# Performance work log

Hardware: AMD Instinct MI355X
Metric: run time of the kernel (lower is better)

Reference implementation:

```python
import jax, jax.numpy as jnp
import numpy as np

PATCH = 16
FEAT = 64
RADIUS = 3
EPS = 1e-06


def setup_inputs() -> dict:
    key = jax.random.key(0)
    ks = jax.random.split(key, 7)
    B, G, H, W, N = 8, 20, 512, 512, 32
    HE = jax.random.uniform(ks[0], (B, 3, H, W), jnp.float32)
    HQST = jax.random.uniform(ks[1], (B, G, H, W), jnp.float32)
    cell_mask = jax.random.randint(ks[2], (B, N, H, W), 0, 2, jnp.int32)
    w1 = jax.random.normal(ks[3], (FEAT, FEAT), jnp.float32) * 0.05
    b1 = jax.random.normal(ks[4], (FEAT,), jnp.float32) * 0.05
    w2 = jax.random.normal(ks[5], (FEAT, FEAT), jnp.float32) * 0.05
    b2 = jax.random.normal(ks[6], (FEAT,), jnp.float32) * 0.05
    return dict(HE=HE, HQST=HQST, cell_mask=cell_mask, w1=w1, b1=b1, w2=w2, b2=b2)


def _select_patch(HE):
    # vectorized per-16x16-patch Shannon entropy + argmax (replaces nested python loops)
    B, _, H, W = HE.shape
    nh, nw = H // PATCH, W // PATCH
    Np = nh * nw
    gray = 0.2989 * HE[:, 0] + 0.587 * HE[:, 1] + 0.114 * HE[:, 2]  # [B,H,W]
    pat = gray.reshape(B, nh, PATCH, nw, PATCH).transpose(0, 1, 3, 2, 4).reshape(B, Np, PATCH * PATCH)
    pat = pat - pat.min(axis=-1, keepdims=True)
    v = pat / (pat.max(axis=-1, keepdims=True) + 1e-08)
    bins = jnp.clip((v * 256.0).astype(jnp.int32), 0, 255)          # 256-bin histc over [0,1]
    flat = (jnp.arange(B * Np, dtype=jnp.int32).reshape(B, Np, 1) * 256 + bins).reshape(-1)
    counts = jnp.zeros(B * Np * 256, jnp.float32).at[flat].add(1.0).reshape(B, Np, 256)
    prob = counts / (counts.sum(axis=-1, keepdims=True) + 1e-08)
    ent = -jnp.sum(jnp.where(prob > 0, prob * jnp.log2(jnp.where(prob > 0, prob, 1.0)), 0.0), axis=-1)
    idx = jnp.argmax(ent, axis=-1)
    return idx // nw, idx % nw


def _corr(X):
    # stabilized cell-cell correlation (detached in the original -> stop_gradient)
    X = X - X.mean(axis=0, keepdims=True)
    X = X / (jnp.std(X, axis=0, keepdims=True, ddof=1) + EPS)
    corr = X @ X.T / (X.shape[1] - 1)
    return jax.lax.stop_gradient(jnp.clip(corr, -1.0, 1.0))


def _ssim(x, y, C1=0.0001, C2=0.0001):
    mu_x, mu_y = x.mean(), y.mean()
    sx, sy = jnp.var(x, ddof=1), jnp.var(y, ddof=1)
    sxy = ((x - mu_x) * (y - mu_y)).mean()
    return (2 * mu_x * mu_y + C1) * (2 * sxy + C2) / ((mu_x ** 2 + mu_y ** 2 + C1) * (sx + sy + C2))


def reference(HE, HQST, cell_mask, w1, b1, w2, b2):
    row, col = _select_patch(HE)  # [B], [B]
    ax = jnp.arange(PATCH, dtype=jnp.float32)

    def per_image(he, hq, mask, r, c):
        y0, x0 = r * PATCH, c * PATCH
        he_c = jax.lax.dynamic_slice(he, (0, y0, x0), (he.shape[0], PATCH, PATCH))
        hq_c = jax.lax.dynamic_slice(hq, (0, y0, x0), (hq.shape[0], PATCH, PATCH))
        m = jax.lax.dynamic_slice(mask, (0, y0, x0), (mask.shape[0], PATCH, PATCH)).astype(jnp.float32)
        mn = m / (m.sum(axis=(1, 2), keepdims=True) + EPS)           # [N,P,P] normalized masks
        E_HE = jnp.einsum('chw,nhw->nc', he_c, mn)                   # [N,3]
        E_HQ = jnp.einsum('ghw,nhw->ng', hq_c, mn)                   # [N,G]
        ind = (m > 0).astype(jnp.float32)
        cnt = ind.sum(axis=(1, 2))
        cx = (ind * ax[None, None, :]).sum(axis=(1, 2)) / cnt        # mean x of nonzero pixels
        cy = (ind * ax[None, :, None]).sum(axis=(1, 2)) / cnt        # mean y
        coords = jnp.stack([cx, cy], axis=1)                         # [N,2]
        d2 = jnp.sum((coords[:, None, :] - coords[None, :, :]) ** 2, axis=-1)
        dist = jnp.sqrt(jnp.maximum(d2, 0.0))
        adj = jnp.exp(-dist / (RADIUS + EPS))
        adj = adj / (adj.sum(axis=1, keepdims=True) + 1e-08)
        pad_he = jnp.pad(E_HE, ((0, 0), (0, FEAT - E_HE.shape[1])))
        pad_hq = jnp.pad(E_HQ, ((0, 0), (0, FEAT - E_HQ.shape[1])))

        def gnn(X):
            h = jax.nn.relu((adj @ X) @ w1.T + b1)
            return jax.nn.relu((adj @ h) @ w2.T + b2)

        f_he = jnp.concatenate([pad_he, gnn(pad_he)], axis=1)        # [N,2*FEAT]
        f_hq = jnp.concatenate([pad_hq, gnn(pad_hq)], axis=1)
        ssim = jnp.clip(_ssim(_corr(f_he), _corr(f_hq)), 0.0, 1.0)
        return 1.0 - ssim

    losses = jax.vmap(per_image)(HE, HQST, cell_mask, row, col)
    return losses.sum() / HE.shape[0]
```

## Files before the change

kernel.cpp:

```cpp
#include <hip/hip_runtime.h>

#define IMG_W   512
#define IMG_HW  (512*512)
#define PATCH   16
#define NPATCH  1024
#define NCELL   32
#define NG      20
#define FEAT    64
#define EPSF    1e-6f

typedef unsigned long long ull;

__device__ __forceinline__ float wave_sum(float v) {
    #pragma unroll
    for (int o = 1; o < 64; o <<= 1) v += __shfl_xor(v, o, 64);
    return v;
}

__device__ __forceinline__ float block_sum(float v, float* sP, int t) {
    #pragma unroll
    for (int o = 1; o < 64; o <<= 1) v += __shfl_xor(v, o, 64);
    __syncthreads();
    if ((t & 63) == 0) sP[t >> 6] = v;
    __syncthreads();
    return sP[0] + sP[1] + sP[2] + sP[3];
}

__global__ __launch_bounds__(256) void k_entropy(const float* __restrict__ HE,
                                                 float* __restrict__ ent) {
    __shared__ int hist[4][256];
    int t = threadIdx.x;
    int w = t >> 6, l = t & 63;
    int pid = blockIdx.x * 4 + w;
    int b  = pid >> 10;
    int p  = pid & 1023;
    int pr = p >> 5, pc = p & 31;
    int r  = l >> 2, q = l & 3;
    size_t base = (size_t)b * 3 * IMG_HW
                + (size_t)(pr * PATCH + r) * IMG_W + pc * PATCH + q * 4;
    float4 cr = *(const float4*)(HE + base);
    float4 cg = *(const float4*)(HE + base + IMG_HW);
    float4 cb = *(const float4*)(HE + base + 2 * IMG_HW);
    float gray[4];
    gray[0] = __fadd_rn(__fadd_rn(__fmul_rn(0.2989f, cr.x), __fmul_rn(0.587f, cg.x)),
                        __fmul_rn(0.114f, cb.x));
    gray[1] = __fadd_rn(__fadd_rn(__fmul_rn(0.2989f, cr.y), __fmul_rn(0.587f, cg.y)),
                        __fmul_rn(0.114f, cb.y));
    gray[2] = __fadd_rn(__fadd_rn(__fmul_rn(0.2989f, cr.z), __fmul_rn(0.587f, cg.z)),
                        __fmul_rn(0.114f, cb.z));
    gray[3] = __fadd_rn(__fadd_rn(__fmul_rn(0.2989f, cr.w), __fmul_rn(0.587f, cg.w)),
                        __fmul_rn(0.114f, cb.w));
    float mn = fminf(fminf(gray[0], gray[1]), fminf(gray[2], gray[3]));
    float mx = fmaxf(fmaxf(gray[0], gray[1]), fmaxf(gray[2], gray[3]));
    #pragma unroll
    for (int o = 1; o < 64; o <<= 1) {
        mn = fminf(mn, __shfl_xor(mn, o, 64));
        mx = fmaxf(mx, __shfl_xor(mx, o, 64));
    }
    float denom = __fadd_rn(__fadd_rn(mx, -mn), 1e-8f);
    int* h = hist[w];
    h[l] = 0; h[l + 64] = 0; h[l + 128] = 0; h[l + 192] = 0;
    #pragma unroll
    for (int j = 0; j < 4; ++j) {
        float v = __fdiv_rn(__fadd_rn(gray[j], -mn), denom);
        int bin = (int)__fmul_rn(v, 256.0f);
        bin = min(max(bin, 0), 255);
        atomicAdd(&h[bin], 1);
    }
    float f[4];
    #pragma unroll
    for (int j = 0; j < 4; ++j) {
        int c = h[l + j * 64];
        float term = 0.0f;
        if (c > 0) {
            float prob = (float)c / 256.0f;
            term = prob * log2f(prob);
        }
        f[j] = term;
    }
    float s = __fadd_rn(__fadd_rn(f[0], f[2]), __fadd_rn(f[1], f[3]));
    #pragma unroll
    for (int o = 32; o >= 1; o >>= 1) s = __fadd_rn(s, __shfl_xor(s, o, 64));
    if (l == 0) ent[pid] = 0.0f - s;
}

__global__ __launch_bounds__(256) void k_argmax(const float* __restrict__ ent,
                                                int* __restrict__ bestp) {
    __shared__ ull sK[4];
    int t = threadIdx.x, b = blockIdx.x;
    ull best = 0ull;
    for (int i = t; i < NPATCH; i += 256) {
        float e = ent[b * NPATCH + i];
        ull k = ((ull)__float_as_uint(e) << 32)
              | (ull)(0xFFFFFFFFu - (unsigned)i);
        best = best > k ? best : k;
    }
    #pragma unroll
    for (int o = 1; o < 64; o <<= 1) {
        ull other = __shfl_xor(best, o, 64);
        best = best > other ? best : other;
    }
    if ((t & 63) == 0) sK[t >> 6] = best;
    __syncthreads();
    if (t == 0) {
        ull key = sK[0];
        #pragma unroll
        for (int wv = 1; wv < 4; ++wv) key = key > sK[wv] ? key : sK[wv];
        bestp[b] = (int)(0xFFFFFFFFu - (unsigned)(key & 0xFFFFFFFFull));
    }
}

__global__ __launch_bounds__(256) void k_moments(
    const float* __restrict__ HE, const float* __restrict__ HQ,
    const int*   __restrict__ M,  const int* __restrict__ bestp,
    float* __restrict__ feat)
{
    __shared__ __align__(16) float sM[256];
    __shared__ float sE[23];
    __shared__ float sP[3][4];
    int t = threadIdx.x;
    int b = blockIdx.x >> 5, n = blockIdx.x & 31;

    unsigned p = (unsigned)bestp[b];
    int y0 = (int)(p >> 5) * PATCH;
    int x0 = (int)(p & 31) * PATCH;
    int py = t >> 4, px = t & 15;
    size_t off = (size_t)(y0 + py) * IMG_W + (x0 + px);

    float mv = (float)M[((size_t)b * NCELL + n) * IMG_HW + off];
    sM[t] = mv;
    int w = t >> 6, lane = t & 63;
    float s0 = wave_sum(mv);
    float s1 = wave_sum(mv * (float)px);
    float s2 = wave_sum(mv * (float)py);
    if (lane == 0) { sP[0][w] = s0; sP[1][w] = s1; sP[2][w] = s2; }
    __syncthreads();

    int r = lane >> 2, q = lane & 3;
    size_t poff = (size_t)(y0 + r) * IMG_W + x0 + q * 4;
    float4 m4 = *(const float4*)&sM[r * 16 + q * 4];
    float part[6];
    #pragma unroll
    for (int kk = 0; kk < 6; ++kk) {
        int c = w + kk * 4;
        part[kk] = 0.0f;
        if (c < 23) {
            const float* cp = (c < 3) ? HE + ((size_t)b * 3 + c) * IMG_HW
                                      : HQ + ((size_t)b * NG + (c - 3)) * IMG_HW;
            float4 v = *(const float4*)(cp + poff);
            part[kk] = v.x * m4.x + v.y * m4.y + v.z * m4.z + v.w * m4.w;
        }
    }
    #pragma unroll
    for (int kk = 0; kk < 6; ++kk) {
        int c = w + kk * 4;
        if (c < 23) {
            float s = wave_sum(part[kk]);
            if (lane == 0) sE[c] = s;
        }
    }
    __syncthreads();
    if (t < 25) {
        float ms = sP[0][0] + sP[0][1] + sP[0][2] + sP[0][3];
        float s;
        if (t == 0)      s = (sP[1][0] + sP[1][1] + sP[1][2] + sP[1][3]) / ms;
        else if (t == 1) s = (sP[2][0] + sP[2][1] + sP[2][2] + sP[2][3]) / ms;
        else             s = sE[t - 2] / (ms + EPSF);
        feat[((size_t)b * 25 + t) * NCELL + n] = s;
    }
}

__global__ __launch_bounds__(256) void k_gnn(
    const float* __restrict__ w1, const float* __restrict__ b1,
    const float* __restrict__ w2, const float* __restrict__ b2,
    const float* __restrict__ feat, float* __restrict__ losses)
{
    __shared__ float sF[2][NCELL * 129];
    __shared__ float sU[4160];
    __shared__ float sAdj[NCELL * 33];
    __shared__ float sCx[32], sCy[32], sRow[32];
    __shared__ float sMu[128], sSd[128];
    __shared__ float sP[4];

    int t = threadIdx.x, b = blockIdx.x;
    const float* fb = feat + (size_t)b * 25 * NCELL;

    if (t < 32) { sCx[t] = fb[t]; sCy[t] = fb[NCELL + t]; }
    for (int i = t; i < 2 * NCELL * 129; i += 256) ((float*)sF)[i] = 0.0f;
    __syncthreads();

    for (int i = t; i < 23 * NCELL; i += 256) {
        int ch = i >> 5, n = i & 31;
        float v = fb[(2 + ch) * NCELL + n];
        if (ch < 3) sF[0][n * 129 + ch]       = v;
        else        sF[1][n * 129 + (ch - 3)] = v;
    }
    for (int i = t; i < NCELL * NCELL; i += 256) {
        int ii = i >> 5, jj = i & 31;
        float dx = sCx[ii] - sCx[jj], dy = sCy[ii] - sCy[jj];
        float dist = sqrtf(fmaxf(dx * dx + dy * dy, 0.0f));
        sAdj[ii * 33 + jj] = expf(-dist / (3.0f + EPSF));
    }
    __syncthreads();
    if (t < 32) {
        float s = 0.0f;
        #pragma unroll
        for (int j = 0; j < 32; ++j) s += sAdj[t * 33 + j];
        sRow[t] = s + 1e-8f;
    }
    __syncthreads();
    for (int i = t; i < NCELL * NCELL; i += 256)
        sAdj[(i >> 5) * 33 + (i & 31)] /= sRow[i >> 5];
    __syncthreads();

    float* sT = sU;
    float* sH = sU + 2080;
    for (int m = 0; m < 2; ++m) {
        float* F = sF[m];
        for (int idx = t; idx < NCELL * FEAT; idx += 256) {
            int n = idx >> 6, f = idx & 63;
            float s = 0.0f;
            #pragma unroll
            for (int k = 0; k < 32; ++k) s += sAdj[n * 33 + k] * F[k * 129 + f];
            sT[n * 65 + f] = s;
        }
        __syncthreads();
        for (int idx = t; idx < NCELL * FEAT; idx += 256) {
            int n = idx >> 6, f = idx & 63;
            const float4* wr = (const float4*)(w1 + (size_t)f * FEAT);
            const float*  tp = &sT[n * 65];
            float s = b1[f];
            #pragma unroll
            for (int k4 = 0; k4 < 16; ++k4) {
                float4 w4 = wr[k4];
                s += tp[k4*4+0]*w4.x + tp[k4*4+1]*w4.y + tp[k4*4+2]*w4.z + tp[k4*4+3]*w4.w;
            }
            sH[n * 65 + f] = fmaxf(s, 0.0f);
        }
        __syncthreads();
        for (int idx = t; idx < NCELL * FEAT; idx += 256) {
            int n = idx >> 6, f = idx & 63;
            float s = 0.0f;
            #pragma unroll
            for (int k = 0; k < 32; ++k) s += sAdj[n * 33 + k] * sH[k * 65 + f];
            sT[n * 65 + f] = s;
        }
        __syncthreads();
        for (int idx = t; idx < NCELL * FEAT; idx += 256) {
            int n = idx >> 6, f = idx & 63;
            const float4* wr = (const float4*)(w2 + (size_t)f * FEAT);
            const float*  tp = &sT[n * 65];
            float s = b2[f];
            #pragma unroll
            for (int k4 = 0; k4 < 16; ++k4) {
                float4 w4 = wr[k4];
                s += tp[k4*4+0]*w4.x + tp[k4*4+1]*w4.y + tp[k4*4+2]*w4.z + tp[k4*4+3]*w4.w;
            }
            F[n * 129 + 64 + f] = fmaxf(s, 0.0f);
        }
        __syncthreads();
    }

    float* sC = sU;
    for (int m = 0; m < 2; ++m) {
        float* F = sF[m];
        if (t < 128) {
            float s = 0.0f;
            #pragma unroll
            for (int n2 = 0; n2 < 32; ++n2) s += F[n2 * 129 + t];
            float mu = s / 32.0f;
            float ss = 0.0f;
            #pragma unroll
            for (int n2 = 0; n2 < 32; ++n2) { float d = F[n2 * 129 + t] - mu; ss += d * d; }
            sMu[t] = mu;
            sSd[t] = sqrtf(ss / 31.0f);
        }
        __syncthreads();
        for (int i = t; i < NCELL * 128; i += 256) {
            int n2 = i >> 7, c = i & 127;
            F[n2 * 129 + c] = (F[n2 * 129 + c] - sMu[c]) / (sSd[c] + EPSF);
        }
        __syncthreads();
        for (int i = t; i < NCELL * NCELL; i += 256) {
            int ii = i >> 5, jj = i & 31;
            float s = 0.0f;
            #pragma unroll
            for (int k = 0; k < 128; ++k) s += F[ii * 129 + k] * F[jj * 129 + k];
            s /= 127.0f;
            sC[m * 1024 + i] = fminf(fmaxf(s, -1.0f), 1.0f);
        }
        __syncthreads();
    }

    float px = 0.0f, py = 0.0f;
    for (int e = t; e < 1024; e += 256) { px += sC[e]; py += sC[1024 + e]; }
    float mux = block_sum(px, sP, t) / 1024.0f;
    float muy = block_sum(py, sP, t) / 1024.0f;
    float va = 0.0f, vb = 0.0f, vc = 0.0f;
    for (int e = t; e < 1024; e += 256) {
        float dx = sC[e] - mux, dy = sC[1024 + e] - muy;
        va += dx * dx; vb += dy * dy; vc += dx * dy;
    }
    float sxv = block_sum(va, sP, t) / 1023.0f;
    float syv = block_sum(vb, sP, t) / 1023.0f;
    float sxy = block_sum(vc, sP, t) / 1024.0f;
    if (t == 0) {
        const float C1 = 1e-4f, C2 = 1e-4f;
        float ssim = (2.0f * mux * muy + C1) * (2.0f * sxy + C2)
                   / ((mux * mux + muy * muy + C1) * (sxv + syv + C2));
        ssim = fminf(fmaxf(ssim, 0.0f), 1.0f);
        losses[b] = 1.0f - ssim;
    }
}

__global__ void k_final(const float* __restrict__ losses, float* __restrict__ out, int B) {
    if (threadIdx.x == 0) {
        float s = 0.0f;
        for (int i = 0; i < B; ++i) s += losses[i];
        out[0] = s / (float)B;
    }
}

extern "C" void kernel_launch(void* const* d_in, const int* in_sizes, int n_in,
                              void* d_out, int out_size, void* d_ws, size_t ws_size,
                              hipStream_t stream) {
    const float* HE = (const float*)d_in[0];
    const float* HQ = (const float*)d_in[1];
    const int*   M  = (const int*)d_in[2];
    const float* w1 = (const float*)d_in[3];
    const float* b1 = (const float*)d_in[4];
    const float* w2 = (const float*)d_in[5];
    const float* b2 = (const float*)d_in[6];
    float* out = (float*)d_out;

    int B = in_sizes[0] / (3 * IMG_HW);

    float* ent    = (float*)d_ws;
    float* losses = (float*)((char*)d_ws + (size_t)B * NPATCH * 4);
    float* feat   = (float*)((char*)losses + (size_t)B * 4);
    int*   bestp  = (int*)((char*)feat + (size_t)B * 25 * NCELL * 4);

    hipLaunchKernelGGL(k_entropy, dim3(B * NPATCH / 4), dim3(256), 0, stream, HE, ent);
    hipLaunchKernelGGL(k_argmax,  dim3(B),              dim3(256), 0, stream, ent, bestp);
    hipLaunchKernelGGL(k_moments, dim3(B * NCELL),      dim3(256), 0, stream, HE, HQ, M, bestp, feat);
    hipLaunchKernelGGL(k_gnn,     dim3(B),              dim3(256), 0, stream, w1, b1, w2, b2, feat, losses);
    hipLaunchKernelGGL(k_final,   dim3(1),              dim3(1),   0, stream, losses, out, B);
}
```

Measured before the change: 440.0 us.

## Fuse argmax, moments, GNN and final reduction into one per-image kernel

```diff
diff --git a/kernel.cpp b/kernel.cpp
--- a/kernel.cpp
+++ b/kernel.cpp
@@ -27,7 +27,9 @@
 }
 
 __global__ __launch_bounds__(256) void k_entropy(const float* __restrict__ HE,
-                                                 float* __restrict__ ent) {
+                                                 float* __restrict__ ent,
+                                                 unsigned* __restrict__ counter) {
+    if (blockIdx.x == 0 && threadIdx.x == 0) *counter = 0u;
     __shared__ int hist[4][256];
     int t = threadIdx.x;
     int w = t >> 6, l = t & 63;
@@ -84,10 +86,26 @@
     if (l == 0) ent[pid] = 0.0f - s;
 }
 
-__global__ __launch_bounds__(256) void k_argmax(const float* __restrict__ ent,
-                                                int* __restrict__ bestp) {
+__global__ __launch_bounds__(256) void k_fused(
+    const float* __restrict__ HE, const float* __restrict__ HQ,
+    const int*   __restrict__ M,  const float* __restrict__ ent,
+    const float* __restrict__ w1, const float* __restrict__ b1,
+    const float* __restrict__ w2, const float* __restrict__ b2,
+    float* __restrict__ losses, unsigned* __restrict__ counter,
+    float* __restrict__ out)
+{
+    __shared__ float sBig[2 * NCELL * 129];
+    __shared__ float sU[4160];
+    __shared__ float sAdj[NCELL * 33];
+    __shared__ float sFeat[25][NCELL];
+    __shared__ float sCx[32], sCy[32], sRow[32];
+    __shared__ float sMu[128], sSd[128];
+    __shared__ float sP[4];
     __shared__ ull sK[4];
+
     int t = threadIdx.x, b = blockIdx.x;
+    int w = t >> 6, lane = t & 63;
+
     ull best = 0ull;
     for (int i = t; i < NPATCH; i += 256) {
         float e = ent[b * NPATCH + i];
@@ -102,96 +120,68 @@
     }
     if ((t & 63) == 0) sK[t >> 6] = best;
     __syncthreads();
-    if (t == 0) {
-        ull key = sK[0];
-        #pragma unroll
-        for (int wv = 1; wv < 4; ++wv) key = key > sK[wv] ? key : sK[wv];
-        bestp[b] = (int)(0xFFFFFFFFu - (unsigned)(key & 0xFFFFFFFFull));
-    }
-}
-
-__global__ __launch_bounds__(256) void k_moments(
-    const float* __restrict__ HE, const float* __restrict__ HQ,
-    const int*   __restrict__ M,  const int* __restrict__ bestp,
-    float* __restrict__ feat)
-{
-    __shared__ __align__(16) float sM[256];
-    __shared__ float sE[23];
-    __shared__ float sP[3][4];
-    int t = threadIdx.x;
-    int b = blockIdx.x >> 5, n = blockIdx.x & 31;
-
-    unsigned p = (unsigned)bestp[b];
+    ull key = sK[0];
+    #pragma unroll
+    for (int wv = 1; wv < 4; ++wv) key = key > sK[wv] ? key : sK[wv];
+    unsigned p = 0xFFFFFFFFu - (unsigned)(key & 0xFFFFFFFFull);
     int y0 = (int)(p >> 5) * PATCH;
     int x0 = (int)(p & 31) * PATCH;
-    int py = t >> 4, px = t & 15;
-    size_t off = (size_t)(y0 + py) * IMG_W + (x0 + px);
-
-    float mv = (float)M[((size_t)b * NCELL + n) * IMG_HW + off];
-    sM[t] = mv;
-    int w = t >> 6, lane = t & 63;
-    float s0 = wave_sum(mv);
-    float s1 = wave_sum(mv * (float)px);
-    float s2 = wave_sum(mv * (float)py);
-    if (lane == 0) { sP[0][w] = s0; sP[1][w] = s1; sP[2][w] = s2; }
-    __syncthreads();
 
     int r = lane >> 2, q = lane & 3;
     size_t poff = (size_t)(y0 + r) * IMG_W + x0 + q * 4;
-    float4 m4 = *(const float4*)&sM[r * 16 + q * 4];
-    float part[6];
+    float* sCh = sBig;
     #pragma unroll
     for (int kk = 0; kk < 6; ++kk) {
         int c = w + kk * 4;
-        part[kk] = 0.0f;
         if (c < 23) {
             const float* cp = (c < 3) ? HE + ((size_t)b * 3 + c) * IMG_HW
                                       : HQ + ((size_t)b * NG + (c - 3)) * IMG_HW;
             float4 v = *(const float4*)(cp + poff);
-            part[kk] = v.x * m4.x + v.y * m4.y + v.z * m4.z + v.w * m4.w;
-        }
-    }
-    #pragma unroll
-    for (int kk = 0; kk < 6; ++kk) {
-        int c = w + kk * 4;
-        if (c < 23) {
-            float s = wave_sum(part[kk]);
-            if (lane == 0) sE[c] = s;
-        }
-    }
-    __syncthreads();
-    if (t < 25) {
-        float ms = sP[0][0] + sP[0][1] + sP[0][2] + sP[0][3];
-        float s;
-        if (t == 0)      s = (sP[1][0] + sP[1][1] + sP[1][2] + sP[1][3]) / ms;
-        else if (t == 1) s = (sP[2][0] + sP[2][1] + sP[2][2] + sP[2][3]) / ms;
-        else             s = sE[t - 2] / (ms + EPSF);
-        feat[((size_t)b * 25 + t) * NCELL + n] = s;
-    }
-}
-
-__global__ __launch_bounds__(256) void k_gnn(
-    const float* __restrict__ w1, const float* __restrict__ b1,
-    const float* __restrict__ w2, const float* __restrict__ b2,
-    const float* __restrict__ feat, float* __restrict__ losses)
-{
-    __shared__ float sF[2][NCELL * 129];
-    __shared__ float sU[4160];
-    __shared__ float sAdj[NCELL * 33];
-    __shared__ float sCx[32], sCy[32], sRow[32];
-    __shared__ float sMu[128], sSd[128];
-    __shared__ float sP[4];
-
-    int t = threadIdx.x, b = blockIdx.x;
-    const float* fb = feat + (size_t)b * 25 * NCELL;
-
-    if (t < 32) { sCx[t] = fb[t]; sCy[t] = fb[NCELL + t]; }
+            *(float4*)&sCh[c * 256 + lane * 4] = v;
+        }
+    }
+
+    int4 mreg[8];
+    #pragma unroll
+    for (int j = 0; j < 8; ++j) {
+        int n = w * 8 + j;
+        const int* mp = M + ((size_t)b * NCELL + n) * IMG_HW + poff;
+        mreg[j] = *(const int4*)mp;
+    }
+    __syncthreads();
+
+    #pragma unroll
+    for (int j = 0; j < 8; ++j) {
+        int n = w * 8 + j;
+        float m0 = (float)mreg[j].x, m1 = (float)mreg[j].y;
+        float m2 = (float)mreg[j].z, m3 = (float)mreg[j].w;
+        float s0 = wave_sum(m0 + m1 + m2 + m3);
+        float fx = (float)(q * 4);
+        float s1 = wave_sum(m0 * fx + m1 * (fx + 1.0f) + m2 * (fx + 2.0f) + m3 * (fx + 3.0f));
+        float s2 = wave_sum((m0 + m1 + m2 + m3) * (float)r);
+        #pragma unroll
+        for (int c = 0; c < 23; ++c) {
+            float4 v = *(const float4*)&sCh[c * 256 + lane * 4];
+            float part = v.x * m0 + v.y * m1 + v.z * m2 + v.w * m3;
+            float s = wave_sum(part);
+            if (lane == 0) sFeat[2 + c][n] = s / (s0 + EPSF);
+        }
+        if (lane == 0) {
+            sFeat[0][n] = s1 / s0;
+            sFeat[1][n] = s2 / s0;
+        }
+    }
+    __syncthreads();
+
+    float (*sF)[NCELL * 129] = (float (*)[NCELL * 129])sBig;
+
+    if (t < 32) { sCx[t] = sFeat[0][t]; sCy[t] = sFeat[1][t]; }
     for (int i = t; i < 2 * NCELL * 129; i += 256) ((float*)sF)[i] = 0.0f;
     __syncthreads();
 
     for (int i = t; i < 23 * NCELL; i += 256) {
         int ch = i >> 5, n = i & 31;
-        float v = fb[(2 + ch) * NCELL + n];
+        float v = sFeat[2 + ch][n];
         if (ch < 3) sF[0][n * 129 + ch]       = v;
         else        sF[1][n * 129 + (ch - 3)] = v;
     }
@@ -309,15 +299,18 @@
         float ssim = (2.0f * mux * muy + C1) * (2.0f * sxy + C2)
                    / ((mux * mux + muy * muy + C1) * (sxv + syv + C2));
         ssim = fminf(fmaxf(ssim, 0.0f), 1.0f);
-        losses[b] = 1.0f - ssim;
-    }
-}
-
-__global__ void k_final(const float* __restrict__ losses, float* __restrict__ out, int B) {
-    if (threadIdx.x == 0) {
-        float s = 0.0f;
-        for (int i = 0; i < B; ++i) s += losses[i];
-        out[0] = s / (float)B;
+        __hip_atomic_store(&losses[b], 1.0f - ssim, __ATOMIC_RELAXED,
+                           __HIP_MEMORY_SCOPE_AGENT);
+        __threadfence();
+        unsigned prev = atomicAdd(counter, 1u);
+        if (prev == (unsigned)(gridDim.x - 1)) {
+            __threadfence();
+            float s = 0.0f;
+            for (int i = 0; i < (int)gridDim.x; ++i)
+                s += __hip_atomic_load(&losses[i], __ATOMIC_RELAXED,
+                                       __HIP_MEMORY_SCOPE_AGENT);
+            out[0] = s / (float)gridDim.x;
+        }
     }
 }
 
@@ -335,14 +328,12 @@
 
     int B = in_sizes[0] / (3 * IMG_HW);
 
-    float* ent    = (float*)d_ws;
-    float* losses = (float*)((char*)d_ws + (size_t)B * NPATCH * 4);
-    float* feat   = (float*)((char*)losses + (size_t)B * 4);
-    int*   bestp  = (int*)((char*)feat + (size_t)B * 25 * NCELL * 4);
-
-    hipLaunchKernelGGL(k_entropy, dim3(B * NPATCH / 4), dim3(256), 0, stream, HE, ent);
-    hipLaunchKernelGGL(k_argmax,  dim3(B),              dim3(256), 0, stream, ent, bestp);
-    hipLaunchKernelGGL(k_moments, dim3(B * NCELL),      dim3(256), 0, stream, HE, HQ, M, bestp, feat);
-    hipLaunchKernelGGL(k_gnn,     dim3(B),              dim3(256), 0, stream, w1, b1, w2, b2, feat, losses);
-    hipLaunchKernelGGL(k_final,   dim3(1),              dim3(1),   0, stream, losses, out, B);
-}
+    float*    ent     = (float*)d_ws;
+    float*    losses  = (float*)((char*)d_ws + (size_t)B * NPATCH * 4);
+    unsigned* counter = (unsigned*)((char*)losses + (size_t)B * 4);
+
+    hipLaunchKernelGGL(k_entropy, dim3(B * NPATCH / 4), dim3(256), 0, stream,
+                       HE, ent, counter);
+    hipLaunchKernelGGL(k_fused,   dim3(B),              dim3(256), 0, stream,
+                       HE, HQ, M, ent, w1, b1, w2, b2, losses, counter, out);
+}
```

Measured after the change: 485.5 us. 10.3% more time.
